# Performance work log

Hardware: AMD Instinct MI355X
Metric: run time of the kernel (lower is better)

The kernel has to match this reference:

```python
import jax, jax.numpy as jnp
import numpy as np

R = 32            # voxel resolution
ALPHA = 0.1       # LeakyReLU slope
BN_EPS = 1e-4     # BatchNormalization epsilon
VOX_EPS = 1e-6    # Voxelization eps (normalize=True)


def _bn_train(x, gamma, beta, axes):
    # training-mode batch norm over `axes`, channel axis = 1
    mean = jnp.mean(x, axes, keepdims=True)
    var = jnp.var(x, axes, keepdims=True)
    bshape = (1, -1) + (1,) * (x.ndim - 2)
    return gamma.reshape(bshape) * (x - mean) * jax.lax.rsqrt(var + BN_EPS) + beta.reshape(bshape)


def _lrelu(x):
    return jnp.where(x >= 0, x, ALPHA * x)


def _voxelize(features, coords):
    # features [B,C,N], coords [B,3,N] -> grid [B,C,R,R,R], norm_coords [B,3,N] in [0,R-1]
    centered = coords - jnp.mean(coords, axis=2, keepdims=True)
    max_norm = jnp.max(jnp.linalg.norm(centered, axis=1, keepdims=True), axis=2, keepdims=True)
    norm = centered / (max_norm * 2.0 + VOX_EPS) + 0.5
    norm = jnp.clip(norm * R, 0.0, R - 1)
    vox = jnp.round(norm).astype(jnp.int32)              # [B,3,N]
    flat = (vox[:, 0] * R + vox[:, 1]) * R + vox[:, 2]   # [B,N]

    def per_batch(f, idx):  # f [C,N], idx [N]
        sums = jax.ops.segment_sum(f.T, idx, num_segments=R ** 3)            # [R^3,C]
        cnt = jax.ops.segment_sum(jnp.ones_like(idx, f.dtype), idx, num_segments=R ** 3)
        return (sums / jnp.maximum(cnt, 1.0)[:, None]).T                      # [C,R^3]

    grid = jax.vmap(per_batch)(features, flat)            # [B,C,R^3]
    B, C = features.shape[0], features.shape[1]
    return grid.reshape(B, C, R, R, R), norm


def _conv3d(x, w, b):
    # x [B,C,D,H,W], w [k,k,k,Cin,Cout], 'same' padding
    y = jax.lax.conv_general_dilated(x, w, (1, 1, 1), 'SAME',
                                     dimension_numbers=('NCDHW', 'DHWIO', 'NCDHW'))
    return y + b.reshape(1, -1, 1, 1, 1)


def _trilinear_devoxelize(vf, coords):
    # vf [B,C,R^3], coords [B,3,N] in [0,R-1] -> [B,C,N]
    c0f = jnp.clip(jnp.floor(coords), 0.0, R - 1)
    frac = coords - c0f                                   # [B,3,N]
    c0 = c0f.astype(jnp.int32)
    c1 = jnp.minimum(c0 + 1, R - 1)
    out = jnp.zeros((vf.shape[0], vf.shape[1], coords.shape[2]), vf.dtype)
    for dx in (0, 1):
        for dy in (0, 1):
            for dz in (0, 1):
                xs = c1[:, 0] if dx else c0[:, 0]
                ys = c1[:, 1] if dy else c0[:, 1]
                zs = c1[:, 2] if dz else c0[:, 2]
                w = ((frac[:, 0] if dx else 1 - frac[:, 0]) *
                     (frac[:, 1] if dy else 1 - frac[:, 1]) *
                     (frac[:, 2] if dz else 1 - frac[:, 2]))           # [B,N]
                idx = (xs * R + ys) * R + zs                            # [B,N]
                g = jnp.take_along_axis(vf, idx[:, None, :], axis=2)    # [B,C,N]
                out = out + w[:, None, :] * g
    return out


def setup_inputs() -> dict:
    key = jax.random.key(0)
    ks = jax.random.split(key, 16)
    B, C, N, K = 8, 64, 16384, 3
    s = 0.05
    return {
        'features': jax.random.normal(ks[0], (B, C, N), jnp.float32),
        'coords': jax.random.normal(ks[1], (B, 3, N), jnp.float32),
        'conv1_w': jax.random.normal(ks[2], (K, K, K, C, C), jnp.float32) * s,
        'conv1_b': jnp.zeros((C,), jnp.float32),
        'bn1_gamma': jnp.ones((C,), jnp.float32),
        'bn1_beta': jnp.zeros((C,), jnp.float32),
        'conv2_w': jax.random.normal(ks[3], (K, K, K, C, C), jnp.float32) * s,
        'conv2_b': jnp.zeros((C,), jnp.float32),
        'bn2_gamma': jnp.ones((C,), jnp.float32),
        'bn2_beta': jnp.zeros((C,), jnp.float32),
        'pf_w': jax.random.normal(ks[4], (C, C), jnp.float32) * s,
        'pf_bias': jnp.zeros((C,), jnp.float32),
        'pf_gamma': jnp.ones((C,), jnp.float32),
        'pf_beta': jnp.zeros((C,), jnp.float32),
    }


def reference(features, coords, conv1_w, conv1_b, bn1_gamma, bn1_beta,
              conv2_w, conv2_b, bn2_gamma, bn2_beta,
              pf_w, pf_bias, pf_gamma, pf_beta):
    vgrid, norm_coords = _voxelize(features, coords)
    v = _lrelu(_bn_train(_conv3d(vgrid, conv1_w, conv1_b), bn1_gamma, bn1_beta, (0, 2, 3, 4)))
    v = _lrelu(_bn_train(_conv3d(v, conv2_w, conv2_b), bn2_gamma, bn2_beta, (0, 2, 3, 4)))
    vflat = v.reshape(v.shape[0], v.shape[1], -1)                 # [B,C,R^3]
    vpts = _trilinear_devoxelize(vflat, norm_coords)              # [B,C,N]
    # point branch: shared MLP (1x1 conv) + BN + LeakyReLU
    p = jnp.einsum('bcn,cd->bdn', features, pf_w) + pf_bias[None, :, None]
    p = _lrelu(_bn_train(p, pf_gamma, pf_beta, (0, 2)))
    return vpts + p, coords
```

## Files before the change

### kernel.cpp

```cpp
#include <hip/hip_runtime.h>
#include <stdint.h>

#define RR 32
#define R3 32768
#define NB 8
#define NCH 64
#define NP 16384

typedef unsigned short u16;
typedef uint32_t u32;
typedef __attribute__((ext_vector_type(8))) short bf8;
typedef __attribute__((ext_vector_type(4))) float f4;
typedef __attribute__((ext_vector_type(16))) float f16x;

#define MFMA(a,b,c)   __builtin_amdgcn_mfma_f32_16x16x32_bf16(a,b,c,0,0,0)
#define MFMA32(a,b,c) __builtin_amdgcn_mfma_f32_32x32x16_bf16(a,b,c,0,0,0)

__device__ __forceinline__ float bf2f(u16 v){
  union { u32 u; float f; } x; x.u = ((u32)v) << 16; return x.f;
}
__device__ __forceinline__ float u2f(u32 u){
  union { u32 u; float f; } x; x.u = u; return x.f;
}
__device__ __forceinline__ u16 f2bf(float f){
  union { float f; u32 u; } x; x.f = f;
  u32 r = x.u + 0x7fffu + ((x.u >> 16) & 1u);
  return (u16)(r >> 16);
}
__device__ __forceinline__ float ldf(const void* p, size_t i, int isbf){
  return isbf ? bf2f(((const u16*)p)[i]) : ((const float*)p)[i];
}

#define OFF_GRID  0ull
#define OFF_BUF1  33554432ull
#define OFF_FT    33554432ull
#define OFF_P     67108864ull
#define OFF_CNT   83886080ull
#define OFF_SMALL 84934656ull
#define OFF_STAT  84936704ull
#define OFF_OFFS  84948992ull
#define OFF_NC    85997568ull
#define OFF_VIDX  87570432ull
#define OFF_SORT  88094720ull
#define OFF_WF1   88619008ull
#define OFF_WF2   88840192ull
#define OFF_WFP   89061376ull
#define WS_NEED   89069568ull
#define ZOFF      OFF_CNT
#define ZBYTES    1062912ull

__global__ void k_dtype(const uint32_t* __restrict__ gamma_raw, int* __restrict__ flag){
  if (threadIdx.x == 0) *flag = (gamma_raw[0] == 0x3F800000u) ? 0 : 1;
}

__global__ void k_coordstats(const void* __restrict__ coords, float* __restrict__ small,
                             const int* __restrict__ dflag){
  int b = blockIdx.x; int tid = threadIdx.x;
  int isbf = *dflag;
  __shared__ float red[1024];
  size_t cb = (size_t)b*3*NP;
  float sx=0.f, sy=0.f, sz=0.f;
  for (int n = tid; n < NP; n += 1024){
    sx += ldf(coords, cb+n, isbf);
    sy += ldf(coords, cb+NP+n, isbf);
    sz += ldf(coords, cb+2*NP+n, isbf);
  }
  float m[3]; float* sums[3] = {&sx,&sy,&sz};
  for (int a = 0; a < 3; a++){
    red[tid] = *sums[a]; __syncthreads();
    for (int s = 512; s > 0; s >>= 1){ if (tid < s) red[tid] += red[tid+s]; __syncthreads(); }
    m[a] = red[0] * (1.0f/NP); __syncthreads();
  }
  float vm = 0.f;
  for (int n = tid; n < NP; n += 1024){
    float cx = ldf(coords, cb+n, isbf)      - m[0];
    float cy = ldf(coords, cb+NP+n, isbf)   - m[1];
    float cz = ldf(coords, cb+2*NP+n, isbf) - m[2];
    vm = fmaxf(vm, sqrtf(cx*cx + cy*cy + cz*cz));
  }
  red[tid] = vm; __syncthreads();
  for (int s = 512; s > 0; s >>= 1){ if (tid < s) red[tid] = fmaxf(red[tid], red[tid+s]); __syncthreads(); }
  if (tid == 0){
    small[384 + b*4 + 0] = m[0];
    small[384 + b*4 + 1] = m[1];
    small[384 + b*4 + 2] = m[2];
    small[384 + b*4 + 3] = 1.0f / (2.0f*red[0] + 1e-6f);
  }
}

__global__ void k_pointprep(const void* __restrict__ coords, const float* __restrict__ small,
                            float* __restrict__ nc, int* __restrict__ vidx, int* __restrict__ cnt,
                            const int* __restrict__ dflag){
  int g = blockIdx.x*256 + threadIdx.x;
  int isbf = *dflag;
  int b = g >> 14; int n = g & (NP-1);
  float mx = small[384+b*4+0], my = small[384+b*4+1], mz = small[384+b*4+2], sc = small[384+b*4+3];
  size_t cb = (size_t)b*3*NP;
  float nx = ((ldf(coords, cb+n, isbf)      - mx)*sc + 0.5f) * 32.0f;
  float ny = ((ldf(coords, cb+NP+n, isbf)   - my)*sc + 0.5f) * 32.0f;
  float nz = ((ldf(coords, cb+2*NP+n, isbf) - mz)*sc + 0.5f) * 32.0f;
  nx = fminf(fmaxf(nx, 0.f), 31.f);
  ny = fminf(fmaxf(ny, 0.f), 31.f);
  nz = fminf(fmaxf(nz, 0.f), 31.f);
  nc[(b*3+0)*NP + n] = nx; nc[(b*3+1)*NP + n] = ny; nc[(b*3+2)*NP + n] = nz;
  int vx = (int)rintf(nx), vy = (int)rintf(ny), vz = (int)rintf(nz);
  int flat = (vx*32 + vy)*32 + vz;
  vidx[g] = flat;
  atomicAdd(&cnt[b*R3 + flat], 1);
}

__global__ void k_scan(const int* __restrict__ cnt, int* __restrict__ off){
  __shared__ int part[1024];
  int b = blockIdx.x, tid = threadIdx.x;
  int base = b*R3 + tid*32;
  int s = 0;
  for (int i = 0; i < 32; i++) s += cnt[base + i];
  part[tid] = s; __syncthreads();
  for (int st = 1; st < 1024; st <<= 1){
    int v = (tid >= st) ? part[tid - st] : 0;
    __syncthreads();
    part[tid] += v;
    __syncthreads();
  }
  int run = (tid == 0) ? 0 : part[tid - 1];
  for (int i = 0; i < 32; i++){ off[base + i] = run; run += cnt[base + i]; }
}

__global__ void k_sortpts(const int* __restrict__ vidx, int* __restrict__ off, int* __restrict__ sorted){
  int g = blockIdx.x*256 + threadIdx.x;
  int b = g >> 14; int n = g & (NP-1);
  int v = vidx[g];
  int slot = atomicAdd(&off[b*R3 + v], 1);
  sorted[b*NP + slot] = n;
}

__global__ void k_voxsum(const u16* __restrict__ fT, const int* __restrict__ sorted,
                         const int* __restrict__ cnt, const int* __restrict__ off,
                         u16* __restrict__ grid){
  int wid = blockIdx.x*4 + (threadIdx.x >> 6);
  int lane = threadIdx.x & 63;
  int b = wid >> 15; int v = wid & (R3-1);
  int cv = cnt[b*R3 + v];
  int end = off[b*R3 + v];
  float acc = 0.f;
  for (int i = end - cv; i < end; i++){
    int n = sorted[b*NP + i];
    acc += bf2f(fT[((size_t)(b*NP + n))*64 + lane]);
  }
  grid[((size_t)(b*R3 + v))*64 + lane] = f2bf(acc / (float)max(cv, 1));
}

__global__ void k_wprep(const void* __restrict__ w, u16* __restrict__ wfrag, const int* __restrict__ dflag){
  int idx = blockIdx.x; int lane = threadIdx.x;
  int isbf = *dflag;
  int ntl = idx & 3; int kk = (idx >> 2) & 1; int tap = idx >> 3;
  int lh = lane & 15, quad = lane >> 4;
  int n = ntl*16 + lh;
  u16* dst = wfrag + ((size_t)idx*64 + lane)*8;
  for (int j = 0; j < 8; j++){
    int k = kk*32 + quad*8 + j;
    dst[j] = f2bf(ldf(w, (size_t)(tap*64 + k)*64 + n, isbf));
  }
}

__global__ void k_wprep32(const void* __restrict__ w, u16* __restrict__ wfrag, const int* __restrict__ dflag){
  int idx = blockIdx.x; int lane = threadIdx.x;
  int isbf = *dflag;
  int nh = idx & 1; int ks = (idx >> 1) & 3; int tap = idx >> 3;
  int n = nh*32 + (lane & 31);
  int khalf = lane >> 5;
  u16* dst = wfrag + ((size_t)idx*64 + lane)*8;
  for (int j = 0; j < 8; j++){
    int cin = ks*16 + khalf*8 + j;
    dst[j] = f2bf(ldf(w, (size_t)(tap*64 + cin)*64 + n, isbf));
  }
}

__device__ __forceinline__ void bn_params(const float* __restrict__ spread, int c, float invM,
                                          float* mean, float* rs){
  float su = 0.f, sq = 0.f;
  #pragma unroll
  for (int i = 0; i < 8; i++){ su += spread[i*128 + c]; sq += spread[i*128 + 64 + c]; }
  float m = su * invM;
  *mean = m;
  *rs = rsqrtf(sq*invM - m*m + 1e-4f);
}

#define PD 6
template<int BN>
__global__ __launch_bounds__(256, 2) void k_conv_t(const u16* __restrict__ in, const u16* __restrict__ wfrag,
                                                   u16* __restrict__ out, const float* __restrict__ spread,
                                                   const void* __restrict__ gamma, const void* __restrict__ beta,
                                                   const int* __restrict__ dflag){
  __shared__ u16 lds_in[16*2176];
  __shared__ float bnA[64], bnB[64];
  int bx = blockIdx.x;
  int b = bx >> 8; int r = bx & 255;
  int u0 = (r >> 4) * 2; int v0 = (r & 15) * 2;
  int tid = threadIdx.x, wv = tid >> 6, lane = tid & 63;

  if constexpr (BN){
    if (tid < 64){
      int isbf = *dflag;
      float mean, rs;
      bn_params(spread, tid, 1.0f/(NB*R3), &mean, &rs);
      float ga = ldf(gamma, tid, isbf), be = ldf(beta, tid, isbf);
      float A = ga*rs;
      bnA[tid] = A; bnB[tid] = be - mean*A;
    }
    __syncthreads();
  }

  uint4 zz; zz.x = 0; zz.y = 0; zz.z = 0; zz.w = 0;
  for (int ri = wv; ri < 16; ri += 4){
    int u2 = u0 + (ri >> 2) - 1;
    int v2 = v0 + (ri & 3) - 1;
    uint4* dstrow = (uint4*)&lds_in[ri*2176];
    if ((unsigned)u2 > 31u || (unsigned)v2 > 31u){
      for (int i = lane; i < 272; i += 64) dstrow[i] = zz;
      continue;
    }
    const uint4* src = (const uint4*)(in + ((size_t)(b*R3 + (u2*32 + v2)*32))*64);
    if (lane < 8) dstrow[lane] = zz;
    else if (lane < 16) dstrow[264 + (lane & 7)] = zz;
    #pragma unroll
    for (int ch = 0; ch < 4; ch++){
      int idx = ch*64 + lane;
      int w = idx >> 3, cc = idx & 7;
      uint4 v = src[idx];
      if constexpr (BN){
        u32 in4[4] = {v.x, v.y, v.z, v.w};
        u32 o4[4];
        #pragma unroll
        for (int k = 0; k < 4; k++){
          int c = cc*8 + 2*k;
          float lo = u2f(in4[k] << 16);
          float hi = u2f(in4[k] & 0xFFFF0000u);
          lo = bnA[c]*lo + bnB[c];     lo = (lo >= 0.f) ? lo : 0.1f*lo;
          hi = bnA[c+1]*hi + bnB[c+1]; hi = (hi >= 0.f) ? hi : 0.1f*hi;
          o4[k] = (u32)f2bf(lo) | ((u32)f2bf(hi) << 16);
        }
        v.x = o4[0]; v.y = o4[1]; v.z = o4[2]; v.w = o4[3];
      }
      int wp = w + 1;
      dstrow[wp*8 + (cc ^ (wp & 7))] = v;
    }
  }
  __syncthreads();

  int nh = wv >> 1, vsel = wv & 1;
  int v_i = v0 + vsel;
  int mlane = lane & 31;
  int khalf = lane >> 5;
  f16x acc0, acc1;
  #pragma unroll
  for (int i = 0; i < 16; i++){ acc0[i] = 0.f; acc1[i] = 0.f; }

  const u16* wstream = wfrag + (size_t)nh*512 + (size_t)lane*8;
  bf8 Wf[PD], A0f[PD], A1f[PD];

  #pragma unroll
  for (int it = 0; it < 108 + PD; ++it){
    if (it >= PD){
      int s = it - PD;
      acc0 = MFMA32(A0f[s % PD], Wf[s % PD], acc0);
      acc1 = MFMA32(A1f[s % PD], Wf[s % PD], acc1);
    }
    if (it < 108){
      int tap = it >> 2, ks = it & 3;
      int dwi = tap % 3, dvi = (tap / 3) % 3, dui = tap / 9;
      const u16* rp = &lds_in[(dui*4 + vsel + dvi)*2176];
      int wp = mlane + dwi;
      int cc = ks*2 + khalf;
      int off = wp*64 + ((cc ^ (wp & 7)) << 3);
      Wf[it % PD]  = *(const bf8*)(wstream + (size_t)it*1024);
      A0f[it % PD] = *(const bf8*)(rp + off);
      A1f[it % PD] = *(const bf8*)(rp + 4*2176 + off);
    }
  }

  int co = nh*32 + mlane;
  int rbase = 4*khalf;
  size_t base0 = ((size_t)(b*R3 + ((u0+0)*32 + v_i)*32))*64;
  size_t base1 = ((size_t)(b*R3 + ((u0+1)*32 + v_i)*32))*64;
  #pragma unroll
  for (int reg = 0; reg < 16; reg++){
    int row = (reg & 3) + 8*(reg >> 2) + rbase;
    out[base0 + (size_t)row*64 + co] = f2bf(acc0[reg]);
    out[base1 + (size_t)row*64 + co] = f2bf(acc1[reg]);
  }
}

__global__ __launch_bounds__(256) void k_stats2(const u16* __restrict__ buf, float* __restrict__ spread, int M){
  __shared__ float sred[4*128];
  int tid = threadIdx.x, bx = blockIdx.x;
  int wv = tid >> 6, lane = tid & 63;
  int sub = lane & 7;
  int g = bx*256 + tid;
  float s[8], s2[8];
  #pragma unroll
  for (int j = 0; j < 8; j++){ s[j] = 0.f; s2[j] = 0.f; }
  const uint4* p4 = (const uint4*)buf;
  size_t total = (size_t)M * 8;
  for (size_t f = g; f < total; f += 262144){
    uint4 v = p4[f];
    u32 ws_[4] = {v.x, v.y, v.z, v.w};
    #pragma unroll
    for (int k = 0; k < 4; k++){
      float lo = u2f(ws_[k] << 16);
      float hi = u2f(ws_[k] & 0xFFFF0000u);
      s[2*k]   += lo; s2[2*k]   += lo*lo;
      s[2*k+1] += hi; s2[2*k+1] += hi*hi;
    }
  }
  #pragma unroll
  for (int j = 0; j < 8; j++){
    #pragma unroll
    for (int m = 8; m <= 32; m <<= 1){
      s[j]  += __shfl_xor(s[j],  m);
      s2[j] += __shfl_xor(s2[j], m);
    }
  }
  if (lane < 8){
    #pragma unroll
    for (int j = 0; j < 8; j++){
      sred[wv*128 + sub*8 + j]      = s[j];
      sred[wv*128 + 64 + sub*8 + j] = s2[j];
    }
  }
  __syncthreads();
  if (tid < 128){
    float t = sred[tid] + sred[128+tid] + sred[256+tid] + sred[384+tid];
    atomicAdd(&spread[(bx & 7)*128 + tid], t);
  }
}

__global__ void k_ftrans(const void* __restrict__ feat, u16* __restrict__ fT, const int* __restrict__ dflag){
  __shared__ u16 t[64*65];
  int bx = blockIdx.x;
  int isbf = *dflag;
  int b = bx >> 8; int n0 = (bx & 255) * 64;
  int tid = threadIdx.x;
  int nl = tid & 63; int cq = tid >> 6;
  for (int cp = 0; cp < 16; cp++){
    int c = cq + cp*4;
    t[c*65 + nl] = f2bf(ldf(feat, ((size_t)(b*NCH + c))*NP + n0 + nl, isbf));
  }
  __syncthreads();
  for (int np2 = 0; np2 < 16; np2++){
    int n = np2*4 + cq; int c = nl;
    fT[((size_t)(b*NP + n0 + n))*64 + c] = t[c*65 + n];
  }
}

__global__ void k_pgemm(const u16* __restrict__ fT, const u16* __restrict__ wfp, u16* __restrict__ p){
  __shared__ u16 As[128*64];
  int bx = blockIdx.x;
  size_t row0 = (size_t)bx * 128;
  int tid = threadIdx.x, wv = tid >> 6, lane = tid & 63;
  const uint4* src = (const uint4*)(fT + row0*64);
  uint4* dst = (uint4*)As;
  for (int i = tid; i < 1024; i += 256) dst[i] = src[i];
  __syncthreads();
  int lh = lane & 15, quad = lane >> 4;
  f4 z4 = {0.f,0.f,0.f,0.f};
  f4 acc[2][4];
  for (int i = 0; i < 2; i++) for (int j = 0; j < 4; j++) acc[i][j] = z4;
  const u16* ap = &As[(wv*32)*64];
  #pragma unroll
  for (int kk = 0; kk < 2; kk++){
    bf8 a0 = *(const bf8*)(ap + lh*64 + kk*32 + quad*8);
    bf8 a1 = *(const bf8*)(ap + (16+lh)*64 + kk*32 + quad*8);
    #pragma unroll
    for (int ntl = 0; ntl < 4; ntl++){
      bf8 bf = *(const bf8*)(wfp + ((size_t)(kk*4 + ntl)*64 + lane)*8);
      acc[0][ntl] = MFMA(a0, bf, acc[0][ntl]);
      acc[1][ntl] = MFMA(a1, bf, acc[1][ntl]);
    }
  }
  #pragma unroll
  for (int mt = 0; mt < 2; mt++)
    for (int ntl = 0; ntl < 4; ntl++)
      for (int reg = 0; reg < 4; reg++){
        int rr = wv*32 + mt*16 + quad*4 + reg;
        p[(row0 + rr)*64 + ntl*16 + lh] = f2bf(acc[mt][ntl][reg]);
      }
}

__global__ void k_devox(const u16* __restrict__ grid, const u16* __restrict__ p,
                        const float* __restrict__ stP, const float* __restrict__ st2,
                        const void* __restrict__ pfg, const void* __restrict__ pfb,
                        const void* __restrict__ g2, const void* __restrict__ b2,
                        const float* __restrict__ nc, void* __restrict__ out0,
                        const int* __restrict__ dflag){
  __shared__ float t[64*65];
  int bx = blockIdx.x;
  int isbf = *dflag;
  int b = bx >> 8; int n0 = (bx & 255) * 64;
  int tid = threadIdx.x, wv = tid >> 6, lane = tid & 63;
  int c = lane;
  float meanP, rsP;
  bn_params(stP, c, 1.0f/(NB*NP), &meanP, &rsP);
  float gaP = ldf(pfg, c, isbf), beP = ldf(pfb, c, isbf);
  float mean2, rs2;
  bn_params(st2, c, 1.0f/(NB*R3), &mean2, &rs2);
  float ga2 = ldf(g2, c, isbf), be2 = ldf(b2, c, isbf);
  float A2 = ga2*rs2, B2 = be2 - mean2*A2;
  for (int pt = wv; pt < 64; pt += 4){
    int n = n0 + pt;
    float nx = nc[(b*3+0)*NP + n];
    float ny = nc[(b*3+1)*NP + n];
    float nz = nc[(b*3+2)*NP + n];
    float x0f = floorf(nx), y0f = floorf(ny), z0f = floorf(nz);
    int x0 = (int)x0f, y0 = (int)y0f, z0 = (int)z0f;
    float fx = nx - x0f, fy = ny - y0f, fz = nz - z0f;
    int x1 = min(x0+1,31), y1 = min(y0+1,31), z1 = min(z0+1,31);
    float acc = 0.f;
    #pragma unroll
    for (int k = 0; k < 8; k++){
      int dx = k >> 2, dy = (k >> 1) & 1, dz = k & 1;
      int xs = dx ? x1 : x0, ys = dy ? y1 : y0, zs = dz ? z1 : z0;
      float wgt = (dx ? fx : 1.f-fx)*(dy ? fy : 1.f-fy)*(dz ? fz : 1.f-fz);
      float gv = bf2f(grid[((size_t)(b*R3 + (xs*32+ys)*32 + zs))*64 + c]);
      gv = A2*gv + B2;
      gv = (gv >= 0.f) ? gv : 0.1f*gv;
      acc += wgt * gv;
    }
    float pv = bf2f(p[((size_t)(b*NP + n))*64 + c]);
    float y = gaP*(pv - meanP)*rsP + beP;
    y = (y >= 0.f) ? y : 0.1f*y;
    t[pt*65 + c] = acc + y;
  }
  __syncthreads();
  for (int cp = 0; cp < 16; cp++){
    int co = wv + cp*4;
    size_t oi = ((size_t)(b*NCH + co))*NP + n0 + lane;
    float val = t[lane*65 + co];
    if (isbf) ((u16*)out0)[oi] = f2bf(val);
    else      ((float*)out0)[oi] = val;
  }
}

__global__ void k_copycoords(const void* __restrict__ coords, void* __restrict__ out0,
                             const int* __restrict__ dflag){
  int g = blockIdx.x*256 + threadIdx.x;
  int isbf = *dflag;
  size_t oi = (size_t)NB*NCH*NP + g;
  if (isbf) ((u16*)out0)[oi]   = ((const u16*)coords)[g];
  else      ((float*)out0)[oi] = ((const float*)coords)[g];
}

extern "C" void kernel_launch(void* const* d_in, const int* in_sizes, int n_in,
                              void* d_out, int out_size, void* d_ws, size_t ws_size,
                              hipStream_t stream){
  if (ws_size < WS_NEED) return;

  const void* feat   = d_in[0];
  const void* coords = d_in[1];
  const void* w1     = d_in[2];
  const void* g1     = d_in[4];
  const void* b1     = d_in[5];
  const void* w2     = d_in[6];
  const void* g2     = d_in[8];
  const void* b2     = d_in[9];
  const void* pw     = d_in[10];
  const void* pg     = d_in[12];
  const void* pb     = d_in[13];

  char* ws = (char*)d_ws;
  u16*   gridv = (u16*)(ws + OFF_GRID);
  u16*   buf1  = (u16*)(ws + OFF_BUF1);
  u16*   fT    = (u16*)(ws + OFF_FT);
  u16*   p     = (u16*)(ws + OFF_P);
  int*   cnt   = (int*)(ws + OFF_CNT);
  float* small = (float*)(ws + OFF_SMALL);
  int*   dflag = (int*)(small + 448);
  float* stat  = (float*)(ws + OFF_STAT);
  int*   offs  = (int*)(ws + OFF_OFFS);
  float* nc    = (float*)(ws + OFF_NC);
  int*   vidx  = (int*)(ws + OFF_VIDX);
  int*   sorted= (int*)(ws + OFF_SORT);
  u16*   wf1   = (u16*)(ws + OFF_WF1);
  u16*   wf2   = (u16*)(ws + OFF_WF2);
  u16*   wfp   = (u16*)(ws + OFF_WFP);

  hipMemsetAsync(ws + ZOFF, 0, ZBYTES, stream);
  k_dtype<<<1, 64, 0, stream>>>((const uint32_t*)g1, dflag);

  k_wprep32<<<27*8, 64, 0, stream>>>(w1, wf1, dflag);
  k_wprep32<<<27*8, 64, 0, stream>>>(w2, wf2, dflag);
  k_wprep<<<8, 64, 0, stream>>>(pw, wfp, dflag);

  k_coordstats<<<NB, 1024, 0, stream>>>(coords, small, dflag);
  k_pointprep<<<NB*NP/256, 256, 0, stream>>>(coords, small, nc, vidx, cnt, dflag);
  k_scan<<<NB, 1024, 0, stream>>>(cnt, offs);
  k_sortpts<<<NB*NP/256, 256, 0, stream>>>(vidx, offs, sorted);

  k_ftrans<<<NB*NP/64, 256, 0, stream>>>(feat, fT, dflag);
  k_voxsum<<<NB*R3/4, 256, 0, stream>>>(fT, sorted, cnt, offs, gridv);
  k_pgemm<<<NB*NP/128, 256, 0, stream>>>(fT, wfp, p);
  k_stats2<<<1024, 256, 0, stream>>>(p, stat + 2048, NB*NP);

  k_conv_t<0><<<NB*256, 256, 0, stream>>>(gridv, wf1, buf1, nullptr, nullptr, nullptr, nullptr);
  k_stats2<<<1024, 256, 0, stream>>>(buf1, stat + 0, NB*R3);

  k_conv_t<1><<<NB*256, 256, 0, stream>>>(buf1, wf2, gridv, stat + 0, g1, b1, dflag);
  k_stats2<<<1024, 256, 0, stream>>>(gridv, stat + 1024, NB*R3);

  k_devox<<<NB*NP/64, 256, 0, stream>>>(gridv, p, stat + 2048, stat + 1024,
                                        pg, pb, g2, b2, nc, d_out, dflag);
  k_copycoords<<<NB*3*NP/256, 256, 0, stream>>>(coords, d_out, dflag);
}
```

Before: 445.4 us.

## Restructure conv MFMA loop into per-tap software pipeline with explicit waitcnt

Replaces the flat 6-deep rolling prefetch over 108 k-steps in the 3x3x3 conv kernel with a per-tap pipeline. Weights are triple-buffered two taps ahead and LDS activations double-buffered one tap ahead. Hand-placed s_waitcnt and sched_barrier instructions control when global and LDS loads must complete before each tap's 8 MFMAs. The goal is to hide global weight load latency and LDS read latency behind MFMA work. The cost is more live registers, which could hurt occupancy under launch_bounds(256,2), and hard-coded wait counts that are fragile if the compiler reorders or splits loads.

Result: faster. 414.2 us (-7.0%).

```diff
diff --git a/kernel.cpp b/kernel.cpp
--- a/kernel.cpp
+++ b/kernel.cpp
@@ -186,7 +186,34 @@
   *rs = rsqrtf(sq*invM - m*m + 1e-4f);
 }
 
-#define PD 6
+#define ISSUE_W(BANK, TAP) do { \
+  _Pragma("unroll") \
+  for (int ks_ = 0; ks_ < 4; ks_++) \
+    BANK[ks_] = *(const bf8*)(wstream + (size_t)((TAP)*4 + ks_)*1024); \
+} while(0)
+
+#define ISSUE_A(B0, B1, TAP) do { \
+  const int t_ = (TAP); \
+  const int dwi_ = t_ % 3, dvi_ = (t_/3) % 3, dui_ = t_/9; \
+  const u16* rp_ = &lds_in[(dui_*4 + vsel + dvi_)*2176]; \
+  const int wp_ = mlane + dwi_; \
+  const int wb_ = wp_*64, wx_ = wp_ & 7; \
+  _Pragma("unroll") \
+  for (int ks_ = 0; ks_ < 4; ks_++){ \
+    const int off_ = wb_ + ((((ks_*2) + khalf) ^ wx_) << 3); \
+    B0[ks_] = *(const bf8*)(rp_ + off_); \
+    B1[ks_] = *(const bf8*)(rp_ + 4*2176 + off_); \
+  } \
+} while(0)
+
+#define CONSUME(BW, B0, B1) do { \
+  _Pragma("unroll") \
+  for (int ks_ = 0; ks_ < 4; ks_++){ \
+    acc0 = MFMA32(B0[ks_], BW[ks_], acc0); \
+    acc1 = MFMA32(B1[ks_], BW[ks_], acc1); \
+  } \
+} while(0)
+
 template<int BN>
 __global__ __launch_bounds__(256, 2) void k_conv_t(const u16* __restrict__ in, const u16* __restrict__ wfrag,
                                                    u16* __restrict__ out, const float* __restrict__ spread,
@@ -257,26 +284,35 @@
   for (int i = 0; i < 16; i++){ acc0[i] = 0.f; acc1[i] = 0.f; }
 
   const u16* wstream = wfrag + (size_t)nh*512 + (size_t)lane*8;
-  bf8 Wf[PD], A0f[PD], A1f[PD];
-
-  #pragma unroll
-  for (int it = 0; it < 108 + PD; ++it){
-    if (it >= PD){
-      int s = it - PD;
-      acc0 = MFMA32(A0f[s % PD], Wf[s % PD], acc0);
-      acc1 = MFMA32(A1f[s % PD], Wf[s % PD], acc1);
-    }
-    if (it < 108){
-      int tap = it >> 2, ks = it & 3;
-      int dwi = tap % 3, dvi = (tap / 3) % 3, dui = tap / 9;
-      const u16* rp = &lds_in[(dui*4 + vsel + dvi)*2176];
-      int wp = mlane + dwi;
-      int cc = ks*2 + khalf;
-      int off = wp*64 + ((cc ^ (wp & 7)) << 3);
-      Wf[it % PD]  = *(const bf8*)(wstream + (size_t)it*1024);
-      A0f[it % PD] = *(const bf8*)(rp + off);
-      A1f[it % PD] = *(const bf8*)(rp + 4*2176 + off);
-    }
+
+  bf8 W0[4], W1[4], W2[4];
+  bf8 Aa0[4], Aa1[4], Ab0[4], Ab1[4];
+
+  ISSUE_W(W0, 0);
+  ISSUE_W(W1, 1);
+  ISSUE_A(Aa0, Aa1, 0);
+
+  #pragma unroll
+  for (int tap = 0; tap < 27; ++tap){
+    const int pf = tap + 2;
+    if (pf < 27){
+      if (pf % 3 == 0)      ISSUE_W(W0, pf);
+      else if (pf % 3 == 1) ISSUE_W(W1, pf);
+      else                  ISSUE_W(W2, pf);
+    }
+    if (tap + 1 < 27){
+      if ((tap + 1) & 1) ISSUE_A(Ab0, Ab1, tap + 1);
+      else               ISSUE_A(Aa0, Aa1, tap + 1);
+    }
+    __builtin_amdgcn_sched_barrier(0);
+    if (tap < 25)       asm volatile("s_waitcnt vmcnt(8) lgkmcnt(8)");
+    else if (tap == 25) asm volatile("s_waitcnt vmcnt(4) lgkmcnt(8)");
+    else                asm volatile("s_waitcnt vmcnt(0) lgkmcnt(0)");
+    __builtin_amdgcn_sched_barrier(0);
+    const int wsel = tap % 3, asel = tap & 1;
+    if (wsel == 0){ if (asel == 0) CONSUME(W0, Aa0, Aa1); else CONSUME(W0, Ab0, Ab1); }
+    else if (wsel == 1){ if (asel == 0) CONSUME(W1, Aa0, Aa1); else CONSUME(W1, Ab0, Ab1); }
+    else              { if (asel == 0) CONSUME(W2, Aa0, Aa1); else CONSUME(W2, Ab0, Ab1); }
   }
 
   int co = nh*32 + mlane;
```
